# Kernel optimization log

Measured on AMD Instinct MI355X. Metric: run time of the kernel, lower is better.

Reference implementation:

```python
import jax, jax.numpy as jnp
import numpy as np

N, E, DIN, DOUT = 10000, 160000, 256, 256
NEG_SLOPE = 0.2
BN_EPS = 1e-5
DROP_P = 0.5


def setup_inputs() -> dict:
    key = jax.random.key(0)
    ks = jax.random.split(key, 12)
    s = 1.0 / np.sqrt(DIN)
    return {
        "x": jax.random.normal(ks[0], (N, DIN), jnp.float32),
        "edge_index": jax.random.randint(ks[1], (2, E), 0, N, jnp.int64),
        "Wl": jax.random.normal(ks[2], (DIN, DOUT), jnp.float32) * s,
        "bl": jax.random.normal(ks[3], (DOUT,), jnp.float32) * s,
        "Wr": jax.random.normal(ks[4], (DIN, DOUT), jnp.float32) * s,
        "br": jax.random.normal(ks[5], (DOUT,), jnp.float32) * s,
        "att": jax.random.normal(ks[6], (DOUT,), jnp.float32) * (1.0 / np.sqrt(DOUT)),
        "bias": jax.random.normal(ks[7], (DOUT,), jnp.float32) * 0.01,
        "gamma": jnp.ones((DOUT,), jnp.float32),
        "beta": jnp.zeros((DOUT,), jnp.float32),
        "dropout_u": jax.random.uniform(ks[8], (N, DOUT), jnp.float32),
    }


def reference(x, edge_index, Wl, bl, Wr, br, att, bias, gamma, beta, dropout_u):
    n = x.shape[0]
    # GATv2Conv (heads=1): separate source/target linear maps
    xl = x @ Wl + bl  # source features [N, DOUT]
    xr = x @ Wr + br  # target features [N, DOUT]
    # add self-loops (PyG default add_self_loops=True)
    loop = jnp.arange(n, dtype=edge_index.dtype)
    src = jnp.concatenate([edge_index[0], loop])  # [E+N]
    dst = jnp.concatenate([edge_index[1], loop])
    # GATv2 attention: e = att . LeakyReLU(xl_j + xr_i)
    h = jax.nn.leaky_relu(xl[src] + xr[dst], NEG_SLOPE)  # [E+N, DOUT]
    alpha = h @ att  # [E+N]
    # segment softmax over destination nodes
    amax = jax.ops.segment_max(alpha, dst, num_segments=n)
    alpha = jnp.exp(alpha - amax[dst])
    denom = jax.ops.segment_sum(alpha, dst, num_segments=n)
    alpha = alpha / denom[dst]
    # scatter-add aggregate of weighted source features
    out = jax.ops.segment_sum(xl[src] * alpha[:, None], dst, num_segments=n)
    out = out + bias
    # ReLU -> dropout(p=0.5, training) -> BatchNorm (training stats)
    out = jax.nn.relu(out)
    mask = (dropout_u >= DROP_P).astype(out.dtype) / (1.0 - DROP_P)
    out = out * mask
    mean = out.mean(axis=0)
    var = out.var(axis=0)  # biased, as BatchNorm uses for normalization
    out = gamma * (out - mean) * jax.lax.rsqrt(var + BN_EPS) + beta
    return out
```

## Files before the change

### kernel.cpp

```cpp
#include <hip/hip_runtime.h>
#include <hip/hip_bf16.h>
#include <math.h>

#define D 256
#define CAP 128
#define NEG_SLOPE 0.2f
#define BN_EPS 1e-5f

typedef __attribute__((ext_vector_type(8))) short bf16x8;
typedef __attribute__((ext_vector_type(8))) unsigned short ushort8;
typedef __attribute__((ext_vector_type(4))) float f32x4;

__device__ inline unsigned short f2bf(float f) {
    union { float f; unsigned u; } v; v.f = f;
    unsigned u = v.u;
    unsigned r = u + 0x7FFFu + ((u >> 16) & 1u);
    return (unsigned short)(r >> 16);
}
__device__ inline float bf2f(unsigned short u) {
    union { unsigned u; float f; } v; v.u = ((unsigned)u) << 16; return v.f;
}

__global__ void prep_kernel(const float* __restrict__ Wl, const float* __restrict__ Wr,
                            int* __restrict__ zero_base, int nzero,
                            unsigned short* __restrict__ Bt) {
    int b = blockIdx.x;
    if (b < 42) {
        int idx = b * 256 + threadIdx.x;
        if (idx < nzero) zero_base[idx] = 0;
    } else {
        int n = b - 42;
        int k = threadIdx.x;
        const float* W = (n < 256) ? Wl : Wr;
        int nn = n & 255;
        Bt[(size_t)n * 256 + k] = f2bf(W[(size_t)k * 256 + nn]);
    }
}

__global__ __launch_bounds__(256) void gemm_scatter_kernel(
    const float* __restrict__ X, const unsigned short* __restrict__ Bt,
    const float* __restrict__ bl, const float* __restrict__ br,
    const int* __restrict__ ei, int* __restrict__ counts, int* __restrict__ ssrc,
    unsigned short* __restrict__ xlbf, float* __restrict__ xr,
    int M, int E, int N, int ngemm)
{
    if ((int)blockIdx.x >= ngemm) {
        int e = (blockIdx.x - ngemm) * 256 + threadIdx.x;
        if (e < E + N) {
            int src, dst;
            if (e < E) { src = ei[e]; dst = ei[E + e]; }
            else       { src = dst = e - E; }
            int pos = atomicAdd(&counts[dst], 1);
            if (pos < CAP) ssrc[dst * CAP + pos] = src;
        }
        return;
    }

    __shared__ __align__(16) unsigned short As[64][136];
    __shared__ __align__(16) unsigned short Bs[64][136];

    const int tid = threadIdx.x;
    const int wave = tid >> 6, lane = tid & 63;
    const int m_l = lane & 15, quad = lane >> 4;
    const int row0 = (blockIdx.x >> 3) * 64;
    const int n0 = (blockIdx.x & 7) * 64;

    f32x4 acc[4] = {};

    for (int k0 = 0; k0 < 256; k0 += 128) {
        __syncthreads();
        #pragma unroll
        for (int i = 0; i < 4; i++) {
            int c = tid + i * 256;
            int r = c >> 4;
            int u = (c & 15) * 8;
            int grow = row0 + r;
            ushort8 av = {0, 0, 0, 0, 0, 0, 0, 0};
            if (grow < M) {
                float4 f0 = *(const float4*)(X + (size_t)grow * 256 + k0 + u);
                float4 f1 = *(const float4*)(X + (size_t)grow * 256 + k0 + u + 4);
                av[0] = f2bf(f0.x); av[1] = f2bf(f0.y);
                av[2] = f2bf(f0.z); av[3] = f2bf(f0.w);
                av[4] = f2bf(f1.x); av[5] = f2bf(f1.y);
                av[6] = f2bf(f1.z); av[7] = f2bf(f1.w);
            }
            *(ushort8*)&As[r][u] = av;
            *(ushort8*)&Bs[r][u] = *(const ushort8*)(Bt + (size_t)(n0 + r) * 256 + k0 + u);
        }
        __syncthreads();

        #pragma unroll
        for (int kk0 = 0; kk0 < 128; kk0 += 32) {
            bf16x8 a = *(const bf16x8*)&As[wave * 16 + m_l][kk0 + quad * 8];
            #pragma unroll
            for (int c = 0; c < 4; c++) {
                bf16x8 b = *(const bf16x8*)&Bs[c * 16 + m_l][kk0 + quad * 8];
                acc[c] = __builtin_amdgcn_mfma_f32_16x16x32_bf16(a, b, acc[c], 0, 0, 0);
            }
        }
    }

    const bool isl = (n0 < 256);
    #pragma unroll
    for (int c = 0; c < 4; c++) {
        int col = n0 + c * 16 + m_l;
        int cc = col & 255;
        float bv = isl ? bl[cc] : br[cc];
        #pragma unroll
        for (int r = 0; r < 4; r++) {
            int row = row0 + wave * 16 + quad * 4 + r;
            if (row < M) {
                float v = acc[c][r] + bv;
                if (isl) xlbf[(size_t)row * 256 + cc] = f2bf(v);
                else     xr[(size_t)row * 256 + cc] = v;
            }
        }
    }
}

__device__ inline float dot8leaky(const float* f, float4 bA, float4 bB,
                                  float4 aA, float4 aB) {
    float h, s = 0.f;
    h = f[0] + bA.x; h = (h > 0.f) ? h : NEG_SLOPE * h; s += h * aA.x;
    h = f[1] + bA.y; h = (h > 0.f) ? h : NEG_SLOPE * h; s += h * aA.y;
    h = f[2] + bA.z; h = (h > 0.f) ? h : NEG_SLOPE * h; s += h * aA.z;
    h = f[3] + bA.w; h = (h > 0.f) ? h : NEG_SLOPE * h; s += h * aA.w;
    h = f[4] + bB.x; h = (h > 0.f) ? h : NEG_SLOPE * h; s += h * aB.x;
    h = f[5] + bB.y; h = (h > 0.f) ? h : NEG_SLOPE * h; s += h * aB.y;
    h = f[6] + bB.z; h = (h > 0.f) ? h : NEG_SLOPE * h; s += h * aB.z;
    h = f[7] + bB.w; h = (h > 0.f) ? h : NEG_SLOPE * h; s += h * aB.w;
    return s;
}

__global__ __launch_bounds__(256) void node_kernel(
    const unsigned short* __restrict__ xlbf, const float* __restrict__ xr,
    const float* __restrict__ att, const float* __restrict__ bias,
    const float* __restrict__ du, const int* __restrict__ counts,
    const int* __restrict__ ssrc, float* __restrict__ out, int N)
{
    const int wave = threadIdx.x >> 6, lane = threadIdx.x & 63;
    const int i = blockIdx.x * 4 + wave;
    if (i >= N) return;
    const int hl = lane & 31;
    const int sid = lane >> 5;

    const float4 attA = ((const float4*)att)[hl * 2];
    const float4 attB = ((const float4*)att)[hl * 2 + 1];
    const float4 bA = ((const float4*)(xr + (size_t)i * D))[hl * 2];
    const float4 bB = ((const float4*)(xr + (size_t)i * D))[hl * 2 + 1];

    int cnt = counts[i];
    if (cnt > CAP) cnt = CAP;
    const int start = i * CAP, end = start + cnt;

    float m = -INFINITY, lsum = 0.f;
    float acc[8] = {0.f, 0.f, 0.f, 0.f, 0.f, 0.f, 0.f, 0.f};
    const ushort8 z8 = {0, 0, 0, 0, 0, 0, 0, 0};

    int e = start + sid;
    ushort8 p0, p1, p2, p3;
    p0 = (e     < end) ? *(const ushort8*)(xlbf + (size_t)ssrc[e]     * D + hl * 8) : z8;
    p1 = (e + 2 < end) ? *(const ushort8*)(xlbf + (size_t)ssrc[e + 2] * D + hl * 8) : z8;
    p2 = (e + 4 < end) ? *(const ushort8*)(xlbf + (size_t)ssrc[e + 4] * D + hl * 8) : z8;
    p3 = (e + 6 < end) ? *(const ushort8*)(xlbf + (size_t)ssrc[e + 6] * D + hl * 8) : z8;

    while (e < end) {
        ushort8 c0 = p0, c1 = p1, c2 = p2, c3 = p3;
        bool v1 = (e + 2 < end), v2 = (e + 4 < end), v3 = (e + 6 < end);
        int en = e + 8;
        p0 = (en     < end) ? *(const ushort8*)(xlbf + (size_t)ssrc[en]     * D + hl * 8) : z8;
        p1 = (en + 2 < end) ? *(const ushort8*)(xlbf + (size_t)ssrc[en + 2] * D + hl * 8) : z8;
        p2 = (en + 4 < end) ? *(const ushort8*)(xlbf + (size_t)ssrc[en + 4] * D + hl * 8) : z8;
        p3 = (en + 6 < end) ? *(const ushort8*)(xlbf + (size_t)ssrc[en + 6] * D + hl * 8) : z8;

        float f0[8], f1[8], f2[8], f3[8];
        #pragma unroll
        for (int k = 0; k < 8; k++) {
            f0[k] = bf2f(c0[k]); f1[k] = bf2f(c1[k]);
            f2[k] = bf2f(c2[k]); f3[k] = bf2f(c3[k]);
        }

        float s0 = dot8leaky(f0, bA, bB, attA, attB);
        float s1 = dot8leaky(f1, bA, bB, attA, attB);
        float s2 = dot8leaky(f2, bA, bB, attA, attB);
        float s3 = dot8leaky(f3, bA, bB, attA, attB);

        #pragma unroll
        for (int off = 1; off < 32; off <<= 1) {
            s0 += __shfl_xor(s0, off);
            s1 += __shfl_xor(s1, off);
            s2 += __shfl_xor(s2, off);
            s3 += __shfl_xor(s3, off);
        }
        if (!v1) s1 = -INFINITY;
        if (!v2) s2 = -INFINITY;
        if (!v3) s3 = -INFINITY;

        float mnew = fmaxf(fmaxf(m, fmaxf(s0, s1)), fmaxf(s2, s3));
        float sc = __expf(m - mnew);
        float e0e = __expf(s0 - mnew);
        float e1e = __expf(s1 - mnew);
        float e2e = __expf(s2 - mnew);
        float e3e = __expf(s3 - mnew);
        lsum = lsum * sc + e0e + e1e + e2e + e3e;
        #pragma unroll
        for (int k = 0; k < 8; k++) {
            acc[k] = acc[k] * sc + e0e * f0[k] + e1e * f1[k]
                                 + e2e * f2[k] + e3e * f3[k];
        }
        m = mnew;
        e = en;
    }

    {
        float mO = __shfl_xor(m, 32);
        float lO = __shfl_xor(lsum, 32);
        float accO[8];
        #pragma unroll
        for (int k = 0; k < 8; k++) accO[k] = __shfl_xor(acc[k], 32);
        float mn = fmaxf(m, mO);
        float wS = (m  == -INFINITY) ? 0.f : __expf(m - mn);
        float wO = (mO == -INFINITY) ? 0.f : __expf(mO - mn);
        lsum = lsum * wS + lO * wO;
        #pragma unroll
        for (int k = 0; k < 8; k++) acc[k] = acc[k] * wS + accO[k] * wO;
    }

    if (lane < 32) {
        float inv = 1.f / lsum;
        float4 biA = ((const float4*)bias)[hl * 2];
        float4 biB = ((const float4*)bias)[hl * 2 + 1];
        float4 uA = ((const float4*)(du + (size_t)i * D))[hl * 2];
        float4 uB = ((const float4*)(du + (size_t)i * D))[hl * 2 + 1];
        float4 oA, oB;
        oA.x = fmaxf(acc[0] * inv + biA.x, 0.f); oA.x = (uA.x >= 0.5f) ? 2.f * oA.x : 0.f;
        oA.y = fmaxf(acc[1] * inv + biA.y, 0.f); oA.y = (uA.y >= 0.5f) ? 2.f * oA.y : 0.f;
        oA.z = fmaxf(acc[2] * inv + biA.z, 0.f); oA.z = (uA.z >= 0.5f) ? 2.f * oA.z : 0.f;
        oA.w = fmaxf(acc[3] * inv + biA.w, 0.f); oA.w = (uA.w >= 0.5f) ? 2.f * oA.w : 0.f;
        oB.x = fmaxf(acc[4] * inv + biB.x, 0.f); oB.x = (uB.x >= 0.5f) ? 2.f * oB.x : 0.f;
        oB.y = fmaxf(acc[5] * inv + biB.y, 0.f); oB.y = (uB.y >= 0.5f) ? 2.f * oB.y : 0.f;
        oB.z = fmaxf(acc[6] * inv + biB.z, 0.f); oB.z = (uB.z >= 0.5f) ? 2.f * oB.z : 0.f;
        oB.w = fmaxf(acc[7] * inv + biB.w, 0.f); oB.w = (uB.w >= 0.5f) ? 2.f * oB.w : 0.f;
        ((float4*)(out + (size_t)i * D))[hl * 2] = oA;
        ((float4*)(out + (size_t)i * D))[hl * 2 + 1] = oB;
    }
}

__global__ void bn_reduce_kernel(const float* __restrict__ pre,
                                 float* __restrict__ colsum,
                                 float* __restrict__ colsumsq, int N) {
    int t = threadIdx.x;
    float s = 0.f, s2 = 0.f;
    for (int r = blockIdx.x; r < N; r += gridDim.x) {
        float v = pre[(size_t)r * D + t];
        s += v; s2 += v * v;
    }
    atomicAdd(&colsum[t], s);
    atomicAdd(&colsumsq[t], s2);
}

__global__ void bn_apply_kernel(float* __restrict__ out,
                                const float* __restrict__ colsum,
                                const float* __restrict__ colsumsq,
                                const float* __restrict__ gamma,
                                const float* __restrict__ beta, int N) {
    int idx4 = blockIdx.x * 256 + threadIdx.x;
    int t0 = (idx4 * 4) & (D - 1);
    float invN = 1.f / (float)N;
    float4 v = ((const float4*)out)[idx4];
    float4 o;
    #pragma unroll
    for (int j = 0; j < 4; j++) {
        float mean = colsum[t0 + j] * invN;
        float var = colsumsq[t0 + j] * invN - mean * mean;
        float r = rsqrtf(var + BN_EPS);
        float vv = (j == 0) ? v.x : (j == 1) ? v.y : (j == 2) ? v.z : v.w;
        float oo = gamma[t0 + j] * (vv - mean) * r + beta[t0 + j];
        if (j == 0) o.x = oo; else if (j == 1) o.y = oo; else if (j == 2) o.z = oo; else o.w = oo;
    }
    ((float4*)out)[idx4] = o;
}

extern "C" void kernel_launch(void* const* d_in, const int* in_sizes, int n_in,
                              void* d_out, int out_size, void* d_ws, size_t ws_size,
                              hipStream_t stream) {
    const float* x     = (const float*)d_in[0];
    const int*   ei    = (const int*)d_in[1];
    const float* Wl    = (const float*)d_in[2];
    const float* bl    = (const float*)d_in[3];
    const float* Wr    = (const float*)d_in[4];
    const float* br    = (const float*)d_in[5];
    const float* att   = (const float*)d_in[6];
    const float* bias  = (const float*)d_in[7];
    const float* gamma = (const float*)d_in[8];
    const float* beta  = (const float*)d_in[9];
    const float* du    = (const float*)d_in[10];

    const int N = in_sizes[0] / D;
    const int E = in_sizes[1] / 2;

    int* ws = (int*)d_ws;
    size_t off = 0;
    float* xr       = (float*)(ws + off); off += (size_t)N * D;
    unsigned short* xlbf = (unsigned short*)(ws + off); off += (size_t)N * D / 2;
    unsigned short* Bt   = (unsigned short*)(ws + off); off += 512 * 256 / 2;
    int*   ssrc     = ws + off;           off += (size_t)N * CAP;
    float* colsum   = (float*)(ws + off); off += D;
    float* colsumsq = (float*)(ws + off); off += D;
    int*   counts   = ws + off;           off += N;
    int nzero = 2 * D + N;

    prep_kernel<<<42 + 512, 256, 0, stream>>>(Wl, Wr, (int*)colsum, nzero, Bt);

    int nMtiles = (N + 63) / 64;
    int ngemm = nMtiles * 8;
    int nscat = (E + N + 255) / 256;
    gemm_scatter_kernel<<<ngemm + nscat, 256, 0, stream>>>(
        x, Bt, bl, br, ei, counts, ssrc, xlbf, xr, N, E, N, ngemm);

    node_kernel<<<(N + 3) / 4, 256, 0, stream>>>(
        xlbf, xr, att, bias, du, counts, ssrc, (float*)d_out, N);

    bn_reduce_kernel<<<256, 256, 0, stream>>>((const float*)d_out, colsum, colsumsq, N);
    bn_apply_kernel<<<(N * D / 4 + 255) / 256, 256, 0, stream>>>(
        (float*)d_out, colsum, colsumsq, gamma, beta, N);
}
```

Before: 166.9 us.

## Fuse BN statistics into node kernel and convert weights inside GEMM

```diff
diff --git a/kernel.cpp b/kernel.cpp
--- a/kernel.cpp
+++ b/kernel.cpp
@@ -21,24 +21,9 @@
     union { unsigned u; float f; } v; v.u = ((unsigned)u) << 16; return v.f;
 }
 
-__global__ void prep_kernel(const float* __restrict__ Wl, const float* __restrict__ Wr,
-                            int* __restrict__ zero_base, int nzero,
-                            unsigned short* __restrict__ Bt) {
-    int b = blockIdx.x;
-    if (b < 42) {
-        int idx = b * 256 + threadIdx.x;
-        if (idx < nzero) zero_base[idx] = 0;
-    } else {
-        int n = b - 42;
-        int k = threadIdx.x;
-        const float* W = (n < 256) ? Wl : Wr;
-        int nn = n & 255;
-        Bt[(size_t)n * 256 + k] = f2bf(W[(size_t)k * 256 + nn]);
-    }
-}
-
 __global__ __launch_bounds__(256) void gemm_scatter_kernel(
-    const float* __restrict__ X, const unsigned short* __restrict__ Bt,
+    const float* __restrict__ X,
+    const float* __restrict__ Wl, const float* __restrict__ Wr,
     const float* __restrict__ bl, const float* __restrict__ br,
     const int* __restrict__ ei, int* __restrict__ counts, int* __restrict__ ssrc,
     unsigned short* __restrict__ xlbf, float* __restrict__ xr,
@@ -64,6 +49,8 @@
     const int m_l = lane & 15, quad = lane >> 4;
     const int row0 = (blockIdx.x >> 3) * 64;
     const int n0 = (blockIdx.x & 7) * 64;
+    const bool isl = (n0 < 256);
+    const float* W = isl ? Wl : Wr;
 
     f32x4 acc[4] = {};
 
@@ -85,7 +72,12 @@
                 av[6] = f2bf(f1.z); av[7] = f2bf(f1.w);
             }
             *(ushort8*)&As[r][u] = av;
-            *(ushort8*)&Bs[r][u] = *(const ushort8*)(Bt + (size_t)(n0 + r) * 256 + k0 + u);
+            int cc = (n0 + r) & 255;
+            ushort8 bv;
+            #pragma unroll
+            for (int j = 0; j < 8; j++)
+                bv[j] = f2bf(W[(size_t)(k0 + u + j) * 256 + cc]);
+            *(ushort8*)&Bs[r][u] = bv;
         }
         __syncthreads();
 
@@ -100,7 +92,6 @@
         }
     }
 
-    const bool isl = (n0 < 256);
     #pragma unroll
     for (int c = 0; c < 4; c++) {
         int col = n0 + c * 16 + m_l;
@@ -136,127 +127,134 @@
     const unsigned short* __restrict__ xlbf, const float* __restrict__ xr,
     const float* __restrict__ att, const float* __restrict__ bias,
     const float* __restrict__ du, const int* __restrict__ counts,
-    const int* __restrict__ ssrc, float* __restrict__ out, int N)
+    const int* __restrict__ ssrc, float* __restrict__ out,
+    float* __restrict__ colsum, float* __restrict__ colsumsq, int N)
 {
-    const int wave = threadIdx.x >> 6, lane = threadIdx.x & 63;
+    const int tid = threadIdx.x;
+    const int wave = tid >> 6, lane = tid & 63;
     const int i = blockIdx.x * 4 + wave;
-    if (i >= N) return;
     const int hl = lane & 31;
     const int sid = lane >> 5;
-
-    const float4 attA = ((const float4*)att)[hl * 2];
-    const float4 attB = ((const float4*)att)[hl * 2 + 1];
-    const float4 bA = ((const float4*)(xr + (size_t)i * D))[hl * 2];
-    const float4 bB = ((const float4*)(xr + (size_t)i * D))[hl * 2 + 1];
-
-    int cnt = counts[i];
-    if (cnt > CAP) cnt = CAP;
-    const int start = i * CAP, end = start + cnt;
-
-    float m = -INFINITY, lsum = 0.f;
-    float acc[8] = {0.f, 0.f, 0.f, 0.f, 0.f, 0.f, 0.f, 0.f};
-    const ushort8 z8 = {0, 0, 0, 0, 0, 0, 0, 0};
-
-    int e = start + sid;
-    ushort8 p0, p1, p2, p3;
-    p0 = (e     < end) ? *(const ushort8*)(xlbf + (size_t)ssrc[e]     * D + hl * 8) : z8;
-    p1 = (e + 2 < end) ? *(const ushort8*)(xlbf + (size_t)ssrc[e + 2] * D + hl * 8) : z8;
-    p2 = (e + 4 < end) ? *(const ushort8*)(xlbf + (size_t)ssrc[e + 4] * D + hl * 8) : z8;
-    p3 = (e + 6 < end) ? *(const ushort8*)(xlbf + (size_t)ssrc[e + 6] * D + hl * 8) : z8;
-
-    while (e < end) {
-        ushort8 c0 = p0, c1 = p1, c2 = p2, c3 = p3;
-        bool v1 = (e + 2 < end), v2 = (e + 4 < end), v3 = (e + 6 < end);
-        int en = e + 8;
-        p0 = (en     < end) ? *(const ushort8*)(xlbf + (size_t)ssrc[en]     * D + hl * 8) : z8;
-        p1 = (en + 2 < end) ? *(const ushort8*)(xlbf + (size_t)ssrc[en + 2] * D + hl * 8) : z8;
-        p2 = (en + 4 < end) ? *(const ushort8*)(xlbf + (size_t)ssrc[en + 4] * D + hl * 8) : z8;
-        p3 = (en + 6 < end) ? *(const ushort8*)(xlbf + (size_t)ssrc[en + 6] * D + hl * 8) : z8;
-
-        float f0[8], f1[8], f2[8], f3[8];
-        #pragma unroll
-        for (int k = 0; k < 8; k++) {
-            f0[k] = bf2f(c0[k]); f1[k] = bf2f(c1[k]);
-            f2[k] = bf2f(c2[k]); f3[k] = bf2f(c3[k]);
-        }
-
-        float s0 = dot8leaky(f0, bA, bB, attA, attB);
-        float s1 = dot8leaky(f1, bA, bB, attA, attB);
-        float s2 = dot8leaky(f2, bA, bB, attA, attB);
-        float s3 = dot8leaky(f3, bA, bB, attA, attB);
-
-        #pragma unroll
-        for (int off = 1; off < 32; off <<= 1) {
-            s0 += __shfl_xor(s0, off);
-            s1 += __shfl_xor(s1, off);
-            s2 += __shfl_xor(s2, off);
-            s3 += __shfl_xor(s3, off);
-        }
-        if (!v1) s1 = -INFINITY;
-        if (!v2) s2 = -INFINITY;
-        if (!v3) s3 = -INFINITY;
-
-        float mnew = fmaxf(fmaxf(m, fmaxf(s0, s1)), fmaxf(s2, s3));
-        float sc = __expf(m - mnew);
-        float e0e = __expf(s0 - mnew);
-        float e1e = __expf(s1 - mnew);
-        float e2e = __expf(s2 - mnew);
-        float e3e = __expf(s3 - mnew);
-        lsum = lsum * sc + e0e + e1e + e2e + e3e;
-        #pragma unroll
-        for (int k = 0; k < 8; k++) {
-            acc[k] = acc[k] * sc + e0e * f0[k] + e1e * f1[k]
-                                 + e2e * f2[k] + e3e * f3[k];
-        }
-        m = mnew;
-        e = en;
-    }
-
-    {
-        float mO = __shfl_xor(m, 32);
-        float lO = __shfl_xor(lsum, 32);
-        float accO[8];
-        #pragma unroll
-        for (int k = 0; k < 8; k++) accO[k] = __shfl_xor(acc[k], 32);
-        float mn = fmaxf(m, mO);
-        float wS = (m  == -INFINITY) ? 0.f : __expf(m - mn);
-        float wO = (mO == -INFINITY) ? 0.f : __expf(mO - mn);
-        lsum = lsum * wS + lO * wO;
-        #pragma unroll
-        for (int k = 0; k < 8; k++) acc[k] = acc[k] * wS + accO[k] * wO;
-    }
-
-    if (lane < 32) {
-        float inv = 1.f / lsum;
-        float4 biA = ((const float4*)bias)[hl * 2];
-        float4 biB = ((const float4*)bias)[hl * 2 + 1];
-        float4 uA = ((const float4*)(du + (size_t)i * D))[hl * 2];
-        float4 uB = ((const float4*)(du + (size_t)i * D))[hl * 2 + 1];
-        float4 oA, oB;
-        oA.x = fmaxf(acc[0] * inv + biA.x, 0.f); oA.x = (uA.x >= 0.5f) ? 2.f * oA.x : 0.f;
-        oA.y = fmaxf(acc[1] * inv + biA.y, 0.f); oA.y = (uA.y >= 0.5f) ? 2.f * oA.y : 0.f;
-        oA.z = fmaxf(acc[2] * inv + biA.z, 0.f); oA.z = (uA.z >= 0.5f) ? 2.f * oA.z : 0.f;
-        oA.w = fmaxf(acc[3] * inv + biA.w, 0.f); oA.w = (uA.w >= 0.5f) ? 2.f * oA.w : 0.f;
-        oB.x = fmaxf(acc[4] * inv + biB.x, 0.f); oB.x = (uB.x >= 0.5f) ? 2.f * oB.x : 0.f;
-        oB.y = fmaxf(acc[5] * inv + biB.y, 0.f); oB.y = (uB.y >= 0.5f) ? 2.f * oB.y : 0.f;
-        oB.z = fmaxf(acc[6] * inv + biB.z, 0.f); oB.z = (uB.z >= 0.5f) ? 2.f * oB.z : 0.f;
-        oB.w = fmaxf(acc[7] * inv + biB.w, 0.f); oB.w = (uB.w >= 0.5f) ? 2.f * oB.w : 0.f;
-        ((float4*)(out + (size_t)i * D))[hl * 2] = oA;
-        ((float4*)(out + (size_t)i * D))[hl * 2 + 1] = oB;
-    }
-}
-
-__global__ void bn_reduce_kernel(const float* __restrict__ pre,
-                                 float* __restrict__ colsum,
-                                 float* __restrict__ colsumsq, int N) {
-    int t = threadIdx.x;
-    float s = 0.f, s2 = 0.f;
-    for (int r = blockIdx.x; r < N; r += gridDim.x) {
-        float v = pre[(size_t)r * D + t];
-        s += v; s2 += v * v;
-    }
-    atomicAdd(&colsum[t], s);
-    atomicAdd(&colsumsq[t], s2);
+    const bool active = (i < N);
+
+    __shared__ float bnsum[256];
+    __shared__ float bnsq[256];
+    bnsum[tid] = 0.f; bnsq[tid] = 0.f;
+    __syncthreads();
+
+    if (active) {
+        const float4 attA = ((const float4*)att)[hl * 2];
+        const float4 attB = ((const float4*)att)[hl * 2 + 1];
+        const float4 bA = ((const float4*)(xr + (size_t)i * D))[hl * 2];
+        const float4 bB = ((const float4*)(xr + (size_t)i * D))[hl * 2 + 1];
+
+        int cnt = counts[i];
+        if (cnt > CAP) cnt = CAP;
+        const int start = i * CAP, end = start + cnt;
+
+        float m = -INFINITY, lsum = 0.f;
+        float acc[8] = {0.f, 0.f, 0.f, 0.f, 0.f, 0.f, 0.f, 0.f};
+        const ushort8 z8 = {0, 0, 0, 0, 0, 0, 0, 0};
+
+        int e = start + sid;
+        ushort8 p0, p1, p2, p3;
+        p0 = (e     < end) ? *(const ushort8*)(xlbf + (size_t)ssrc[e]     * D + hl * 8) : z8;
+        p1 = (e + 2 < end) ? *(const ushort8*)(xlbf + (size_t)ssrc[e + 2] * D + hl * 8) : z8;
+        p2 = (e + 4 < end) ? *(const ushort8*)(xlbf + (size_t)ssrc[e + 4] * D + hl * 8) : z8;
+        p3 = (e + 6 < end) ? *(const ushort8*)(xlbf + (size_t)ssrc[e + 6] * D + hl * 8) : z8;
+
+        while (e < end) {
+            ushort8 c0 = p0, c1 = p1, c2 = p2, c3 = p3;
+            bool v1 = (e + 2 < end), v2 = (e + 4 < end), v3 = (e + 6 < end);
+            int en = e + 8;
+            p0 = (en     < end) ? *(const ushort8*)(xlbf + (size_t)ssrc[en]     * D + hl * 8) : z8;
+            p1 = (en + 2 < end) ? *(const ushort8*)(xlbf + (size_t)ssrc[en + 2] * D + hl * 8) : z8;
+            p2 = (en + 4 < end) ? *(const ushort8*)(xlbf + (size_t)ssrc[en + 4] * D + hl * 8) : z8;
+            p3 = (en + 6 < end) ? *(const ushort8*)(xlbf + (size_t)ssrc[en + 6] * D + hl * 8) : z8;
+
+            float f0[8], f1[8], f2[8], f3[8];
+            #pragma unroll
+            for (int k = 0; k < 8; k++) {
+                f0[k] = bf2f(c0[k]); f1[k] = bf2f(c1[k]);
+                f2[k] = bf2f(c2[k]); f3[k] = bf2f(c3[k]);
+            }
+
+            float s0 = dot8leaky(f0, bA, bB, attA, attB);
+            float s1 = dot8leaky(f1, bA, bB, attA, attB);
+            float s2 = dot8leaky(f2, bA, bB, attA, attB);
+            float s3 = dot8leaky(f3, bA, bB, attA, attB);
+
+            #pragma unroll
+            for (int off = 1; off < 32; off <<= 1) {
+                s0 += __shfl_xor(s0, off);
+                s1 += __shfl_xor(s1, off);
+                s2 += __shfl_xor(s2, off);
+                s3 += __shfl_xor(s3, off);
+            }
+            if (!v1) s1 = -INFINITY;
+            if (!v2) s2 = -INFINITY;
+            if (!v3) s3 = -INFINITY;
+
+            float mnew = fmaxf(fmaxf(m, fmaxf(s0, s1)), fmaxf(s2, s3));
+            float sc = __expf(m - mnew);
+            float e0e = __expf(s0 - mnew);
+            float e1e = __expf(s1 - mnew);
+            float e2e = __expf(s2 - mnew);
+            float e3e = __expf(s3 - mnew);
+            lsum = lsum * sc + e0e + e1e + e2e + e3e;
+            #pragma unroll
+            for (int k = 0; k < 8; k++) {
+                acc[k] = acc[k] * sc + e0e * f0[k] + e1e * f1[k]
+                                     + e2e * f2[k] + e3e * f3[k];
+            }
+            m = mnew;
+            e = en;
+        }
+
+        {
+            float mO = __shfl_xor(m, 32);
+            float lO = __shfl_xor(lsum, 32);
+            float accO[8];
+            #pragma unroll
+            for (int k = 0; k < 8; k++) accO[k] = __shfl_xor(acc[k], 32);
+            float mn = fmaxf(m, mO);
+            float wS = (m  == -INFINITY) ? 0.f : __expf(m - mn);
+            float wO = (mO == -INFINITY) ? 0.f : __expf(mO - mn);
+            lsum = lsum * wS + lO * wO;
+            #pragma unroll
+            for (int k = 0; k < 8; k++) acc[k] = acc[k] * wS + accO[k] * wO;
+        }
+
+        if (lane < 32) {
+            float inv = 1.f / lsum;
+            float4 biA = ((const float4*)bias)[hl * 2];
+            float4 biB = ((const float4*)bias)[hl * 2 + 1];
+            float4 uA = ((const float4*)(du + (size_t)i * D))[hl * 2];
+            float4 uB = ((const float4*)(du + (size_t)i * D))[hl * 2 + 1];
+            float o[8];
+            o[0] = fmaxf(acc[0] * inv + biA.x, 0.f); o[0] = (uA.x >= 0.5f) ? 2.f * o[0] : 0.f;
+            o[1] = fmaxf(acc[1] * inv + biA.y, 0.f); o[1] = (uA.y >= 0.5f) ? 2.f * o[1] : 0.f;
+            o[2] = fmaxf(acc[2] * inv + biA.z, 0.f); o[2] = (uA.z >= 0.5f) ? 2.f * o[2] : 0.f;
+            o[3] = fmaxf(acc[3] * inv + biA.w, 0.f); o[3] = (uA.w >= 0.5f) ? 2.f * o[3] : 0.f;
+            o[4] = fmaxf(acc[4] * inv + biB.x, 0.f); o[4] = (uB.x >= 0.5f) ? 2.f * o[4] : 0.f;
+            o[5] = fmaxf(acc[5] * inv + biB.y, 0.f); o[5] = (uB.y >= 0.5f) ? 2.f * o[5] : 0.f;
+            o[6] = fmaxf(acc[6] * inv + biB.z, 0.f); o[6] = (uB.z >= 0.5f) ? 2.f * o[6] : 0.f;
+            o[7] = fmaxf(acc[7] * inv + biB.w, 0.f); o[7] = (uB.w >= 0.5f) ? 2.f * o[7] : 0.f;
+            float4 oA = make_float4(o[0], o[1], o[2], o[3]);
+            float4 oB = make_float4(o[4], o[5], o[6], o[7]);
+            ((float4*)(out + (size_t)i * D))[hl * 2] = oA;
+            ((float4*)(out + (size_t)i * D))[hl * 2 + 1] = oB;
+            #pragma unroll
+            for (int k = 0; k < 8; k++) {
+                atomicAdd(&bnsum[hl * 8 + k], o[k]);
+                atomicAdd(&bnsq[hl * 8 + k], o[k] * o[k]);
+            }
+        }
+    }
+
+    __syncthreads();
+    atomicAdd(&colsum[tid], bnsum[tid]);
+    atomicAdd(&colsumsq[tid], bnsq[tid]);
 }
 
 __global__ void bn_apply_kernel(float* __restrict__ out,
@@ -303,25 +301,24 @@
     size_t off = 0;
     float* xr       = (float*)(ws + off); off += (size_t)N * D;
     unsigned short* xlbf = (unsigned short*)(ws + off); off += (size_t)N * D / 2;
-    unsigned short* Bt   = (unsigned short*)(ws + off); off += 512 * 256 / 2;
     int*   ssrc     = ws + off;           off += (size_t)N * CAP;
     float* colsum   = (float*)(ws + off); off += D;
     float* colsumsq = (float*)(ws + off); off += D;
     int*   counts   = ws + off;           off += N;
-    int nzero = 2 * D + N;
-
-    prep_kernel<<<42 + 512, 256, 0, stream>>>(Wl, Wr, (int*)colsum, nzero, Bt);
+
+    size_t zero_bytes = (size_t)(2 * D + N) * sizeof(int);
+    hipMemsetAsync(colsum, 0, zero_bytes, stream);
 
     int nMtiles = (N + 63) / 64;
     int ngemm = nMtiles * 8;
     int nscat = (E + N + 255) / 256;
     gemm_scatter_kernel<<<ngemm + nscat, 256, 0, stream>>>(
-        x, Bt, bl, br, ei, counts, ssrc, xlbf, xr, N, E, N, ngemm);
+        x, Wl, Wr, bl, br, ei, counts, ssrc, xlbf, xr, N, E, N, ngemm);
 
     node_kernel<<<(N + 3) / 4, 256, 0, stream>>>(
-        xlbf, xr, att, bias, du, counts, ssrc, (float*)d_out, N);
-
-    bn_reduce_kernel<<<256, 256, 0, stream>>>((const float*)d_out, colsum, colsumsq, N);
+        xlbf, xr, att, bias, du, counts, ssrc, (float*)d_out,
+        colsum, colsumsq, N);
+
     bn_apply_kernel<<<(N * D / 4 + 255) / 256, 256, 0, stream>>>(
         (float*)d_out, colsum, colsumsq, gamma, beta, N);
 }
```

Result: slower. 227.7 us (+36.4%).
